# Kernel tuning notes

Measured on AMD Instinct MI355X. Metric: run time of the kernel, lower is better.

## Reference

```python
import jax, jax.numpy as jnp
import numpy as np

B, T = 32, 64
C, H, W = 1, 32, 32
A, E, D, S, HID = 2, 64, 128, 32, 128
K, STRIDE, PAD = 4, 2, 1
FEAT = 64 * 4 * 4  # conv stack output: 64 channels at 4x4


def _lin(x, w, b):
    return x @ w.T + b


def _conv(x, w, b):
    y = jax.lax.conv_general_dilated(x, w, (STRIDE, STRIDE), [(PAD, PAD)] * 2,
                                     dimension_numbers=('NCHW', 'OIHW', 'NCHW'))
    return y + b[None, :, None, None]


def _deconv(x, w, b):
    # torch ConvTranspose2d(w: (in_c,out_c,k,k), stride=2, pad=1) as dilated conv
    w_ = jnp.flip(w, (2, 3)).transpose(1, 0, 2, 3)
    p = K - 1 - PAD
    y = jax.lax.conv_general_dilated(x, w_, (1, 1), [(p, p)] * 2,
                                     lhs_dilation=(STRIDE, STRIDE),
                                     dimension_numbers=('NCHW', 'OIHW', 'NCHW'))
    return y + b[None, :, None, None]


def _mlp(x, w1, b1, w2, b2, w3, b3):
    h = jax.nn.elu(_lin(x, w1, b1))
    h = jax.nn.elu(_lin(h, w2, b2))
    out = _lin(h, w3, b3)
    return out[..., :S], jnp.clip(out[..., S:], -5.0, 2.0)


def _gru(x, h, wih, whh, bih, bhh):
    # torch nn.GRUCell semantics
    gi = x @ wih.T + bih
    gh = h @ whh.T + bhh
    ir, iz, inn = jnp.split(gi, 3, -1)
    hr, hz, hn = jnp.split(gh, 3, -1)
    r = jax.nn.sigmoid(ir + hr)
    u = jax.nn.sigmoid(iz + hz)
    n = jnp.tanh(inn + r * hn)
    return (1.0 - u) * n + u * h


def setup_inputs():
    keys = iter(jax.random.split(jax.random.key(0), 64))

    def p(shape, fan):
        return jax.random.normal(next(keys), shape, jnp.float32) / np.sqrt(fan)

    return dict(
        obs=jax.random.normal(next(keys), (B, T, C, H, W), jnp.float32),
        actions=jax.random.normal(next(keys), (B, T, A), jnp.float32),
        noise=jax.random.normal(next(keys), (T, B, S), jnp.float32),
        enc_w1=p((32, C, K, K), C * K * K), enc_b1=jnp.zeros(32),
        enc_w2=p((64, 32, K, K), 32 * K * K), enc_b2=jnp.zeros(64),
        enc_w3=p((64, 64, K, K), 64 * K * K), enc_b3=jnp.zeros(64),
        enc_pw=p((E, FEAT), FEAT), enc_pb=jnp.zeros(E),
        dec_pw=p((FEAT, D + S), D + S), dec_pb=jnp.zeros(FEAT),
        dec_w1=p((64, 64, K, K), 64 * K * K), dec_b1=jnp.zeros(64),
        dec_w2=p((64, 32, K, K), 64 * K * K), dec_b2=jnp.zeros(32),
        dec_w3=p((32, C, K, K), 32 * K * K), dec_b3=jnp.zeros(C),
        gru_wih=p((3 * D, S + A), D), gru_whh=p((3 * D, D), D),
        gru_bih=jnp.zeros(3 * D), gru_bhh=jnp.zeros(3 * D),
        pri_w1=p((HID, D + A), D + A), pri_b1=jnp.zeros(HID),
        pri_w2=p((HID, HID), HID), pri_b2=jnp.zeros(HID),
        pri_w3=p((2 * S, HID), HID), pri_b3=jnp.zeros(2 * S),
        pos_w1=p((HID, D + E), D + E), pos_b1=jnp.zeros(HID),
        pos_w2=p((HID, HID), HID), pos_b2=jnp.zeros(HID),
        pos_w3=p((2 * S, HID), HID), pos_b3=jnp.zeros(2 * S),
    )


def reference(obs, actions, noise, enc_w1, enc_b1, enc_w2, enc_b2, enc_w3, enc_b3,
              enc_pw, enc_pb, dec_pw, dec_pb, dec_w1, dec_b1, dec_w2, dec_b2,
              dec_w3, dec_b3, gru_wih, gru_whh, gru_bih, gru_bhh,
              pri_w1, pri_b1, pri_w2, pri_b2, pri_w3, pri_b3,
              pos_w1, pos_b1, pos_w2, pos_b2, pos_w3, pos_b3):
    Bq, Tq = obs.shape[:2]
    # --- CNN encoder over all frames at once ---
    x = obs.reshape(Bq * Tq, C, H, W)
    x = jax.nn.relu(_conv(x, enc_w1, enc_b1))
    x = jax.nn.relu(_conv(x, enc_w2, enc_b2))
    x = jax.nn.relu(_conv(x, enc_w3, enc_b3))
    embed = _lin(x.reshape(Bq * Tq, -1), enc_pw, enc_pb).reshape(Bq, Tq, E)

    # --- sequential RSSM core (use_posterior=True path) ---
    def step(h, inp):
        a, e_t, eps = inp
        pm, pls = _mlp(jnp.concatenate([h, e_t], -1),
                       pos_w1, pos_b1, pos_w2, pos_b2, pos_w3, pos_b3)
        z = pm + jnp.exp(pls) * eps
        prm, prls = _mlp(jnp.concatenate([h, a], -1),
                         pri_w1, pri_b1, pri_w2, pri_b2, pri_w3, pri_b3)
        h_new = _gru(jnp.concatenate([z, a], -1), h, gru_wih, gru_whh, gru_bih, gru_bhh)
        return h_new, (z, prm, prls, pm, pls, h)  # h = pre-update (used for decode)

    h0 = jnp.zeros((Bq, D), obs.dtype)
    h_final, (zs, prm, prls, pm, pls, hs) = jax.lax.scan(
        step, h0, (actions.swapaxes(0, 1), embed.swapaxes(0, 1), noise))

    # --- batched decode of all (h_t, z_t); same math as per-step decode ---
    hz = jnp.concatenate([hs, zs], -1).reshape(Tq * Bq, D + S)
    y = _lin(hz, dec_pw, dec_pb).reshape(Tq * Bq, 64, 4, 4)
    y = jax.nn.relu(_deconv(y, dec_w1, dec_b1))
    y = jax.nn.relu(_deconv(y, dec_w2, dec_b2))
    y = jax.nn.sigmoid(_deconv(y, dec_w3, dec_b3))
    recons = y.reshape(Tq, Bq, C, H, W).swapaxes(0, 1)

    tb = lambda t: t.swapaxes(0, 1)  # (T,B,.) -> (B,T,.)
    return (recons, tb(zs), tb(prm), tb(prls), tb(pm), tb(pls), h_final)
```

## Files before the change

### kernel.cpp

```cpp
#include <hip/hip_runtime.h>
#include <math.h>

#define NB 32
#define NT 64
#define NF 2048

#define OUT_ZS    2097152
#define OUT_PRM   (OUT_ZS + 65536)
#define OUT_PRLS  (OUT_PRM + 65536)
#define OUT_PM    (OUT_PRLS + 65536)
#define OUT_PLS   (OUT_PM + 65536)
#define OUT_HF    (OUT_PLS + 65536)

#define WS_HS    27394048
#define WS_ENCT  27656192
#define WS_DECT  27721728
#define WS_WP1H  27885568
#define WS_WP2   27893760
#define WS_WP3   27901952
#define WS_WWHH  27906048
#define WS_WIHZ  27930624
#define WS_QW1T  27936768
#define WS_QW2T  27953408
#define WS_QW3T  27969792
#define WS_PW1T  27977984
#define WS_WIHT  28002560
#define WS_WC2   16777216
#define WS_WC3   (WS_WC2 + 16384)
#define WS_WD1   (WS_WC3 + 32768)
#define WS_WD2   (WS_WD1 + 32768)
#define WS_POSL1E 25165824
#define WS_GIA    (WS_POSL1E + 262144)

typedef __attribute__((ext_vector_type(8))) short short8;
typedef __attribute__((ext_vector_type(4))) float floatx4;
typedef _Float16 __attribute__((ext_vector_type(2))) half2v;
union U4S8 { uint4 u; short8 s; };
__device__ __forceinline__ short8 u2s(uint4 u) { U4S8 x; x.u = u; return x.s; }
__device__ __forceinline__ float eluf(float a) { return (a > 0.f) ? a : expm1f(a); }
__device__ __forceinline__ float sigm(float a) { return 1.f / (1.f + expf(-a)); }
__device__ __forceinline__ unsigned short f2bf(float f) {
  unsigned int u = __float_as_uint(f);
  u += 0x7fffu + ((u >> 16) & 1u);
  return (unsigned short)(u >> 16);
}
__device__ __forceinline__ unsigned short f2h(float f) {
  _Float16 h = (_Float16)f;
  return __builtin_bit_cast(unsigned short, h);
}
union UH2 { unsigned int u; half2v h; };
__device__ __forceinline__ half2v u2h(unsigned int u) { UH2 x; x.u = u; return x.h; }

__device__ __forceinline__ float fdot2w(half2v a, half2v b, float c) {
#if __has_builtin(__builtin_amdgcn_fdot2)
  return __builtin_amdgcn_fdot2(a, b, c, false);
#else
  return fmaf((float)a[0], (float)b[0], fmaf((float)a[1], (float)b[1], c));
#endif
}

union U4H2 { uint4 u; half2v h[4]; };
__device__ __forceinline__ void dot8h(uint4 w, uint4 x,
                                      float& a0, float& a1, float& a2, float& a3) {
  U4H2 W; W.u = w;
  U4H2 X; X.u = x;
  a0 = fdot2w(W.h[0], X.h[0], a0);
  a1 = fdot2w(W.h[1], X.h[1], a1);
  a2 = fdot2w(W.h[2], X.h[2], a2);
  a3 = fdot2w(W.h[3], X.h[3], a3);
}

struct PP { const float* src; void* dst; int n; int mode; int A; int B; };
struct PPAll { PP m[16]; };

__global__ __launch_bounds__(256) void k_prep(PPAll a) {
  PP p = a.m[blockIdx.y];
  for (int i = blockIdx.x * 256 + threadIdx.x; i < p.n; i += gridDim.x * 256) {
    if (p.mode == 10) {
      const int r = i / p.B, c = i - r * p.B;
      ((float*)p.dst)[c * p.A + r] = p.src[i];
    } else {
      float v;
      if (p.mode == 0) v = p.src[i];
      else if (p.mode == 1) v = p.src[(i >> 7) * 192 + (i & 127)];
      else if (p.mode == 2) v = p.src[(i >> 5) * 34 + (i & 31)];
      else if (p.mode == 5) {
        const int kq = i >> 12, o = (i >> 2) & 1023, kl = (i >> 1) & 1, h = i & 1;
        v = p.src[o * 160 + kq * 4 + kl * 2 + h];
      } else {
        const int ab = p.A * p.B;
        const int t = i / ab, rem = i - t * ab;
        const int oc = rem / p.B, ic = rem - oc * p.B;
        v = (p.mode == 3) ? p.src[(oc * p.B + ic) * 16 + t]
                          : p.src[(ic * p.A + oc) * 16 + t];
      }
      ((unsigned short*)p.dst)[i] = (p.mode <= 2 || p.mode == 5) ? f2h(v) : f2bf(v);
    }
  }
}

__global__ __launch_bounds__(256, 2) void k_enc(
    const float* __restrict__ obs, const float* __restrict__ act,
    const float* __restrict__ w1, const float* __restrict__ b1,
    const unsigned short* __restrict__ wc2, const float* __restrict__ b2,
    const unsigned short* __restrict__ wc3, const float* __restrict__ b3,
    const float* __restrict__ encT, const float* __restrict__ encb,
    const float* __restrict__ pw1T, const float* __restrict__ pb1,
    const float* __restrict__ wihT, const float* __restrict__ bih,
    float* __restrict__ posl1e, float* __restrict__ gia) {
  const int f = blockIdx.x, tid = threadIdx.x;
  const int w = tid >> 6, l = tid & 63, q = l >> 4, n = l & 15;
  __shared__ float sIn1[32 * 33];
  __shared__ float sW1[512];
  __shared__ float sB1[32];
  __shared__ __align__(16) unsigned short sIn2[18 * 18 * 40];
  __shared__ __align__(16) unsigned short sIn3[10 * 10 * 72];
  __shared__ __align__(16) float sXe[1024];
  __shared__ float sP[256];
  __shared__ float sE[64];
  __shared__ float sA2[2];

  {
    const float* in = obs + (size_t)f * 1024;
    for (int i = tid; i < 1024; i += 256) sIn1[(i >> 5) * 33 + (i & 31)] = in[i];
    for (int i = tid; i < 512; i += 256) sW1[i] = w1[i];
    if (tid < 32) sB1[tid] = b1[tid];
    if (tid < 2) sA2[tid] = act[(size_t)f * 2 + tid];
    unsigned int* z2 = (unsigned int*)sIn2;
    for (int i = tid; i < 18 * 18 * 40 / 2; i += 256) z2[i] = 0u;
    unsigned int* z3 = (unsigned int*)sIn3;
    for (int i = tid; i < 10 * 10 * 72 / 2; i += 256) z3[i] = 0u;
  }
  __syncthreads();
  for (int r = tid; r < 512; r += 256) {
    const int oc = r >> 4, oy = r & 15;
    float acc[16];
    const float bv = sB1[oc];
#pragma unroll
    for (int j = 0; j < 16; j++) acc[j] = bv;
#pragma unroll
    for (int ky = 0; ky < 4; ky++) {
      const int iy = 2 * oy + ky - 1;
      if (iy < 0 || iy >= 32) continue;
#pragma unroll
      for (int kx = 0; kx < 4; kx++) {
        const float wv = sW1[oc * 16 + ky * 4 + kx];
#pragma unroll
        for (int j = 0; j < 16; j++) {
          const int ix = 2 * j + kx - 1;
          if (ix >= 0 && ix < 32) acc[j] += wv * sIn1[iy * 33 + ix];
        }
      }
    }
#pragma unroll
    for (int j = 0; j < 16; j++)
      sIn2[((oy + 1) * 18 + (j + 1)) * 40 + oc] = f2bf(fmaxf(acc[j], 0.f));
  }
  __syncthreads();
  {
    int base[4];
#pragma unroll
    for (int nt = 0; nt < 4; nt++) {
      const int px = nt * 16 + n, oy = px >> 3, ox = px & 7;
      base[nt] = ((2 * oy + 1) * 18 + (2 * ox + 1)) * 40 + q * 8;
    }
    floatx4 acc[4];
#pragma unroll
    for (int nt = 0; nt < 4; nt++) acc[nt] = (floatx4){0.f, 0.f, 0.f, 0.f};
    uint4 af[16];
#pragma unroll
    for (int t = 0; t < 16; t++)
      af[t] = *reinterpret_cast<const uint4*>(wc2 + (size_t)(t * 64 + w * 16 + n) * 32 + q * 8);
#pragma unroll
    for (int t = 0; t < 16; t++) {
      const int toff = ((t / 4 - 1) * 18 + (t % 4 - 1)) * 40;
#pragma unroll
      for (int nt = 0; nt < 4; nt++) {
        uint4 bf = *reinterpret_cast<const uint4*>(&sIn2[base[nt] + toff]);
        acc[nt] = __builtin_amdgcn_mfma_f32_16x16x32_bf16(u2s(af[t]), u2s(bf), acc[nt], 0, 0, 0);
      }
    }
    float b4[4];
#pragma unroll
    for (int r = 0; r < 4; r++) b4[r] = b2[w * 16 + q * 4 + r];
    __syncthreads();
#pragma unroll
    for (int nt = 0; nt < 4; nt++) {
      const int px = nt * 16 + n, oy = px >> 3, ox = px & 7;
#pragma unroll
      for (int r = 0; r < 4; r++)
        sIn3[((oy + 1) * 10 + (ox + 1)) * 72 + (w * 16 + q * 4 + r)] =
            f2bf(fmaxf(acc[nt][r] + b4[r], 0.f));
    }
  }
  __syncthreads();
  {
    const int oy = n >> 2, ox = n & 3;
    const int ibase = ((2 * oy + 1) * 10 + (2 * ox + 1)) * 72 + q * 8;
    floatx4 acc = (floatx4){0.f, 0.f, 0.f, 0.f};
    for (int ks = 0; ks < 2; ks++) {
      uint4 af[16];
#pragma unroll
      for (int t = 0; t < 16; t++)
        af[t] = *reinterpret_cast<const uint4*>(
            wc3 + (size_t)(t * 64 + w * 16 + n) * 64 + ks * 32 + q * 8);
#pragma unroll
      for (int t = 0; t < 16; t++) {
        const int toff = ((t / 4 - 1) * 10 + (t % 4 - 1)) * 72 + ks * 32;
        uint4 bf = *reinterpret_cast<const uint4*>(&sIn3[ibase + toff]);
        acc = __builtin_amdgcn_mfma_f32_16x16x32_bf16(u2s(af[t]), u2s(bf), acc, 0, 0, 0);
      }
    }
#pragma unroll
    for (int r = 0; r < 4; r++) {
      const int ch = w * 16 + q * 4 + r;
      sXe[ch * 16 + n] = fmaxf(acc[r] + b3[ch], 0.f);
    }
  }
  __syncthreads();
  {
    const int o = tid & 63, s = tid >> 6;
    float acc = 0.f;
    const int k0 = s * 256;
    for (int k = k0; k < k0 + 256; k++) acc += encT[k * 64 + o] * sXe[k];
    sP[tid] = acc;
  }
  __syncthreads();
  if (tid < 64)
    sE[tid] = sP[tid] + sP[tid + 64] + sP[tid + 128] + sP[tid + 192] + encb[tid];
  __syncthreads();
  if (tid < 128) {
    float a = pb1[tid];
    for (int k = 0; k < 64; k++) a += pw1T[(128 + k) * 128 + tid] * sE[k];
    posl1e[(size_t)f * 128 + tid] = a;
  } else {
#pragma unroll
    for (int jj = 0; jj < 3; jj++) {
      const int j = (tid - 128) + jj * 128;
      gia[(size_t)f * 384 + j] =
          bih[j] + wihT[32 * 384 + j] * sA2[0] + wihT[33 * 384 + j] * sA2[1];
    }
  }
}

__global__ __launch_bounds__(512, 2) void k_rssm4(
    const float* __restrict__ posl1e, const float* __restrict__ gia,
    const float* __restrict__ noise,
    const unsigned short* __restrict__ wp1h, const unsigned short* __restrict__ wp2,
    const unsigned short* __restrict__ wp3, const unsigned short* __restrict__ wwhh,
    const unsigned short* __restrict__ wihz,
    const float* __restrict__ pb2, const float* __restrict__ pb3,
    const float* __restrict__ bhh,
    float* __restrict__ hs, float* __restrict__ out) {
  const int b = blockIdx.x, tid = threadIdx.x;
  __shared__ __align__(16) _Float16 sHh[128];
  __shared__ __align__(16) _Float16 sL1h[128];
  __shared__ __align__(16) _Float16 sL2h[128];
  __shared__ __align__(16) _Float16 sZh[32];
  __shared__ float sGh[384];
  __shared__ float sPM[64];

  uint4 wA[16];
  {
    const unsigned short* rowA =
        (tid < 128) ? (wp1h + tid * 128) : (wwhh + (size_t)(tid - 128) * 128);
#pragma unroll
    for (int i = 0; i < 16; i++) wA[i] = reinterpret_cast<const uint4*>(rowA)[i];
  }
  uint4 wB[4];
  {
    const unsigned short* rowB = wp2 + (tid >> 2) * 128 + (tid & 3) * 32;
#pragma unroll
    for (int i = 0; i < 4; i++) wB[i] = reinterpret_cast<const uint4*>(rowB)[i];
  }
  uint4 wC[2];
  {
    const unsigned short* rowC = wp3 + (tid >> 3) * 128 + (tid & 7) * 16;
#pragma unroll
    for (int i = 0; i < 2; i++) wC[i] = reinterpret_cast<const uint4*>(rowC)[i];
  }
  uint4 wD[3][4];
  if (tid < 128) {
#pragma unroll
    for (int j = 0; j < 3; j++) {
      const unsigned short* rowD = wihz + (size_t)(tid + 128 * j) * 32;
#pragma unroll
      for (int i = 0; i < 4; i++) wD[j][i] = reinterpret_cast<const uint4*>(rowD)[i];
    }
  }
  const float bhhR = (tid >= 128) ? bhh[tid - 128] : 0.f;
  const float pb2R = pb2[tid >> 2];
  const float pb3mR = (tid < 32) ? pb3[tid] : 0.f;
  const float pb3sR = (tid < 32) ? pb3[tid + 32] : 0.f;

  float h_reg = 0.f;
  float pl1R = 0.f, gaR0 = 0.f, gaR1 = 0.f, gaR2 = 0.f, epsR = 0.f;
  if (tid < 128) {
    pl1R = posl1e[(size_t)(b * 64) * 128 + tid];
    const size_t gb = (size_t)(b * 64) * 384 + tid;
    gaR0 = gia[gb];
    gaR1 = gia[gb + 128];
    gaR2 = gia[gb + 256];
    sHh[tid] = (_Float16)0.f;
    hs[(size_t)b * 128 + tid] = 0.f;
  }
  if (tid < 32) epsR = noise[(size_t)b * 32 + tid];
  __syncthreads();

  for (int t = 0; t < 64; ++t) {
    const int tn = (t < 63) ? t + 1 : 63;
    float pl1N = 0.f, gaN0 = 0.f, gaN1 = 0.f, gaN2 = 0.f, epsN = 0.f;
    if (tid < 128) {
      pl1N = posl1e[(size_t)(b * 64 + tn) * 128 + tid];
      const size_t gb = (size_t)(b * 64 + tn) * 384 + tid;
      gaN0 = gia[gb];
      gaN1 = gia[gb + 128];
      gaN2 = gia[gb + 256];
    }
    if (tid < 32) epsN = noise[(size_t)(tn * 32 + b) * 32 + tid];

    {
      float a0 = 0.f, a1 = 0.f, a2 = 0.f, a3 = 0.f;
      const uint4* xs = reinterpret_cast<const uint4*>(sHh);
#pragma unroll
      for (int g = 0; g < 16; g++) dot8h(wA[g], xs[g], a0, a1, a2, a3);
      const float a = (a0 + a1) + (a2 + a3);
      if (tid < 128) sL1h[tid] = (_Float16)eluf(a + pl1R);
      else sGh[tid - 128] = a + bhhR;
    }
    __syncthreads();
    {
      float a0 = 0.f, a1 = 0.f, a2 = 0.f, a3 = 0.f;
      const uint4* xs = reinterpret_cast<const uint4*>(sL1h) + (tid & 3) * 4;
#pragma unroll
      for (int i = 0; i < 4; i++) dot8h(wB[i], xs[i], a0, a1, a2, a3);
      float p = (a0 + a1) + (a2 + a3);
      p += __shfl_xor(p, 1);
      p += __shfl_xor(p, 2);
      if ((tid & 3) == 0) sL2h[tid >> 2] = (_Float16)eluf(p + pb2R);
    }
    __syncthreads();
    {
      float a0 = 0.f, a1 = 0.f, a2 = 0.f, a3 = 0.f;
      const uint4* xs = reinterpret_cast<const uint4*>(sL2h) + (tid & 7) * 2;
      dot8h(wC[0], xs[0], a0, a1, a2, a3);
      dot8h(wC[1], xs[1], a0, a1, a2, a3);
      float p = (a0 + a1) + (a2 + a3);
      p += __shfl_xor(p, 1);
      p += __shfl_xor(p, 2);
      p += __shfl_xor(p, 4);
      if ((tid & 7) == 0) sPM[tid >> 3] = p;
    }
    __syncthreads();
    if (tid < 32) {
      const float pm = sPM[tid] + pb3mR;
      float pls = sPM[32 + tid] + pb3sR;
      pls = fminf(fmaxf(pls, -5.f), 2.f);
      const float z = pm + expf(pls) * epsR;
      sZh[tid] = (_Float16)z;
      const int o = (b * 64 + t) * 32 + tid;
      out[OUT_ZS + o] = z;
      out[OUT_PM + o] = pm;
      out[OUT_PLS + o] = pls;
    }
    __syncthreads();
    if (tid < 128) {
      float r0 = 0.f, r1 = 0.f, r2 = 0.f, r3 = 0.f;
      float u0 = 0.f, u1 = 0.f, u2 = 0.f, u3 = 0.f;
      float m0 = 0.f, m1 = 0.f, m2 = 0.f, m3 = 0.f;
      const uint4* xs = reinterpret_cast<const uint4*>(sZh);
#pragma unroll
      for (int i = 0; i < 4; i++) {
        const uint4 xv = xs[i];
        dot8h(wD[0][i], xv, r0, r1, r2, r3);
        dot8h(wD[1][i], xv, u0, u1, u2, u3);
        dot8h(wD[2][i], xv, m0, m1, m2, m3);
      }
      const float gr = gaR0 + ((r0 + r1) + (r2 + r3));
      const float gu = gaR1 + ((u0 + u1) + (u2 + u3));
      const float gn = gaR2 + ((m0 + m1) + (m2 + m3));
      const float r = sigm(gr + sGh[tid]);
      const float u = sigm(gu + sGh[128 + tid]);
      const float n = tanhf(gn + r * sGh[256 + tid]);
      const float hn = (1.f - u) * n + u * h_reg;
      h_reg = hn;
      sHh[tid] = (_Float16)hn;
      if (t < 63) hs[(size_t)((t + 1) * 32 + b) * 128 + tid] = hn;
    }
    pl1R = pl1N;
    gaR0 = gaN0;
    gaR1 = gaN1;
    gaR2 = gaN2;
    epsR = epsN;
    __syncthreads();
  }
  if (tid < 128) out[OUT_HF + b * 128 + tid] = h_reg;
}

__global__ __launch_bounds__(128) void k_pri(const float* __restrict__ hs,
    const float* __restrict__ act,
    const float* __restrict__ qw1T, const float* __restrict__ qb1,
    const float* __restrict__ qw2T, const float* __restrict__ qb2,
    const float* __restrict__ qw3T, const float* __restrict__ qb3,
    float* __restrict__ out) {
  __shared__ float sV[128], sW[128];
  __shared__ float sA2[2];
  const int f = blockIdx.x, tid = threadIdx.x;
  const int t = f >> 5, b = f & 31;
  sV[tid] = hs[(size_t)f * 128 + tid];
  if (tid < 2) sA2[tid] = act[(size_t)(b * 64 + t) * 2 + tid];
  __syncthreads();
  {
    float a = qb1[tid];
    for (int k = 0; k < 128; k++) a += qw1T[k * 128 + tid] * sV[k];
    a += qw1T[128 * 128 + tid] * sA2[0] + qw1T[129 * 128 + tid] * sA2[1];
    sW[tid] = eluf(a);
  }
  __syncthreads();
  {
    float a = qb2[tid];
    for (int k = 0; k < 128; k++) a += qw2T[k * 128 + tid] * sW[k];
    sV[tid] = eluf(a);
  }
  __syncthreads();
  if (tid < 64) {
    float a = qb3[tid];
    for (int k = 0; k < 128; k++) a += qw3T[k * 64 + tid] * sV[k];
    const int o = (b * 64 + t) * 32;
    if (tid < 32) out[OUT_PRM + o + tid] = a;
    else out[OUT_PRLS + o + tid - 32] = fminf(fmaxf(a, -5.f), 2.f);
  }
}

__global__ __launch_bounds__(256, 4) void k_dec(
    const float* __restrict__ hs, const float* __restrict__ zs,
    const unsigned short* __restrict__ decTh, const float* __restrict__ decb,
    const unsigned short* __restrict__ wd1, const float* __restrict__ db1,
    const unsigned short* __restrict__ wd2, const float* __restrict__ db2,
    const float* __restrict__ w3, const float* __restrict__ b3,
    float* __restrict__ out) {
  const int f = blockIdx.x, tid = threadIdx.x;
  const int w = tid >> 6, l = tid & 63, q = l >> 4, n = l & 15;
  const int t = f >> 5, b = f & 31;
  __shared__ __align__(16) _Float16 sXh[160];
  __shared__ __align__(16) unsigned short sInD1[6 * 6 * 72];
  __shared__ __align__(16) unsigned short sInD2[10 * 10 * 72];
  __shared__ __align__(16) _Float16 sInD3h[16 * 16 * 32];
  __shared__ __align__(16) _Float16 sW3h[16 * 32];

  if (tid < 128) sXh[tid] = (_Float16)hs[(size_t)f * 128 + tid];
  else if (tid < 160) sXh[tid] = (_Float16)zs[(size_t)(b * 64 + t) * 32 + (tid - 128)];
  {
    unsigned int* z1 = (unsigned int*)sInD1;
    for (int i = tid; i < 6 * 6 * 72 / 2; i += 256) z1[i] = 0u;
    unsigned int* z2 = (unsigned int*)sInD2;
    for (int i = tid; i < 10 * 10 * 72 / 2; i += 256) z2[i] = 0u;
    for (int s = tid; s < 512; s += 256) {
      const int tap = s >> 5, icc = s & 31;
      sW3h[s] = (_Float16)w3[icc * 16 + tap];
    }
  }
  __syncthreads();
  {
    float acA[4] = {0.f, 0.f, 0.f, 0.f};
    float acB[4] = {0.f, 0.f, 0.f, 0.f};
    const uint2* dT = reinterpret_cast<const uint2*>(decTh);
    const unsigned int* xh = reinterpret_cast<const unsigned int*>(sXh);
#pragma unroll 2
    for (int kq = 0; kq < 40; kq++) {
      const half2v x0 = u2h(xh[2 * kq]);
      const half2v x1 = u2h(xh[2 * kq + 1]);
#pragma unroll
      for (int i = 0; i < 4; i++) {
        const uint2 wv = dT[kq * 1024 + i * 256 + tid];
        acA[i] = fdot2w(u2h(wv.x), x0, acA[i]);
        acB[i] = fdot2w(u2h(wv.y), x1, acB[i]);
      }
    }
#pragma unroll
    for (int i = 0; i < 4; i++) {
      const int o = i * 256 + tid, c = o >> 4, px = o & 15;
      const int Y = px >> 2, X = px & 3;
      sInD1[((Y + 1) * 6 + (X + 1)) * 72 + c] = f2bf(acA[i] + acB[i] + decb[o]);
    }
  }
  __syncthreads();
  {
    const int Y = n >> 2, X = n & 3;
    const int ibase = ((Y + 1) * 6 + (X + 1)) * 72 + q * 8;
    float b4[4];
#pragma unroll
    for (int r = 0; r < 4; r++) b4[r] = db1[w * 16 + q * 4 + r];
#pragma unroll
    for (int c = 0; c < 4; c++) {
      const int cy = c >> 1, cx = c & 1;
      floatx4 acc = (floatx4){0.f, 0.f, 0.f, 0.f};
      for (int ks = 0; ks < 2; ks++) {
        uint4 af[4];
#pragma unroll
        for (int tt = 0; tt < 4; tt++) {
          const int t2 = tt >> 1, t3 = tt & 1;
          const int ky = ((cy + 1) & 1) + 2 * t2, kx = ((cx + 1) & 1) + 2 * t3;
          af[tt] = *reinterpret_cast<const uint4*>(
              wd1 + (size_t)((ky * 4 + kx) * 64 + w * 16 + n) * 64 + ks * 32 + q * 8);
        }
#pragma unroll
        for (int tt = 0; tt < 4; tt++) {
          const int t2 = tt >> 1, t3 = tt & 1;
          const int toff = ((cy - t2) * 6 + (cx - t3)) * 72 + ks * 32;
          uint4 bf = *reinterpret_cast<const uint4*>(&sInD1[ibase + toff]);
          acc = __builtin_amdgcn_mfma_f32_16x16x32_bf16(u2s(af[tt]), u2s(bf), acc, 0, 0, 0);
        }
      }
      const int oy = 2 * Y + cy, ox = 2 * X + cx;
#pragma unroll
      for (int r = 0; r < 4; r++)
        sInD2[((oy + 1) * 10 + (ox + 1)) * 72 + (w * 16 + q * 4 + r)] =
            f2bf(fmaxf(acc[r] + b4[r], 0.f));
    }
  }
  __syncthreads();
  {
    const int px = w * 16 + n;
    const int Y = px >> 3, X = px & 7;
    const int ibase = ((Y + 1) * 10 + (X + 1)) * 72 + q * 8;
    float b4[2][4];
#pragma unroll
    for (int mi = 0; mi < 2; mi++)
#pragma unroll
      for (int r = 0; r < 4; r++) b4[mi][r] = db2[mi * 16 + q * 4 + r];
#pragma unroll
    for (int c = 0; c < 4; c++) {
      const int cy = c >> 1, cx = c & 1;
      floatx4 acc[2];
      acc[0] = (floatx4){0.f, 0.f, 0.f, 0.f};
      acc[1] = (floatx4){0.f, 0.f, 0.f, 0.f};
      for (int ks = 0; ks < 2; ks++) {
        uint4 af[2][4];
#pragma unroll
        for (int mi = 0; mi < 2; mi++)
#pragma unroll
          for (int tt = 0; tt < 4; tt++) {
            const int t2 = tt >> 1, t3 = tt & 1;
            const int ky = ((cy + 1) & 1) + 2 * t2, kx = ((cx + 1) & 1) + 2 * t3;
            af[mi][tt] = *reinterpret_cast<const uint4*>(
                wd2 + (size_t)((ky * 4 + kx) * 32 + mi * 16 + n) * 64 + ks * 32 + q * 8);
          }
#pragma unroll
        for (int tt = 0; tt < 4; tt++) {
          const int t2 = tt >> 1, t3 = tt & 1;
          const int toff = ((cy - t2) * 10 + (cx - t3)) * 72 + ks * 32;
          uint4 bf = *reinterpret_cast<const uint4*>(&sInD2[ibase + toff]);
#pragma unroll
          for (int mi = 0; mi < 2; mi++)
            acc[mi] = __builtin_amdgcn_mfma_f32_16x16x32_bf16(u2s(af[mi][tt]), u2s(bf),
                                                              acc[mi], 0, 0, 0);
        }
      }
      const int oy = 2 * Y + cy, ox = 2 * X + cx;
#pragma unroll
      for (int mi = 0; mi < 2; mi++) {
        const unsigned int lo =
            (unsigned int)f2h(fmaxf(acc[mi][0] + b4[mi][0], 0.f)) |
            ((unsigned int)f2h(fmaxf(acc[mi][1] + b4[mi][1], 0.f)) << 16);
        const unsigned int hi =
            (unsigned int)f2h(fmaxf(acc[mi][2] + b4[mi][2], 0.f)) |
            ((unsigned int)f2h(fmaxf(acc[mi][3] + b4[mi][3], 0.f)) << 16);
        *reinterpret_cast<uint2*>(&sInD3h[(oy * 16 + ox) * 32 + mi * 16 + q * 4]) =
            make_uint2(lo, hi);
      }
    }
  }
  __syncthreads();
  {
    const int oy = tid >> 3;
    const int rem2 = tid & 7;
    const int cpar = rem2 >> 2, qq = rem2 & 3;
    const int py = (oy + 1) & 1, pc = (cpar + 1) & 1;
    float acc[4] = {0.f, 0.f, 0.f, 0.f};
    const float bv = b3[0];
#pragma unroll
    for (int u2 = 0; u2 < 2; u2++) {
      const int ky = py + 2 * u2;
      const int iy = (oy + 1 - ky) >> 1;
      if (iy < 0 || iy >= 16) continue;
#pragma unroll
      for (int u3 = 0; u3 < 2; u3++) {
        const int kx = pc + 2 * u3;
        const int ixb = (cpar + 1 - kx) >> 1;
        const uint4* wv = reinterpret_cast<const uint4*>(&sW3h[(ky * 4 + kx) * 32]);
        const uint4 w0 = wv[0], w1 = wv[1], w2 = wv[2], w3v = wv[3];
#pragma unroll
        for (int j = 0; j < 4; j++) {
          const int ix = ixb + qq * 4 + j;
          if (ix < 0 || ix >= 16) continue;
          const uint4* xp = reinterpret_cast<const uint4*>(&sInD3h[(iy * 16 + ix) * 32]);
          float a0 = 0.f, a1 = 0.f, a2 = 0.f, a3 = 0.f;
          dot8h(w0, xp[0], a0, a1, a2, a3);
          dot8h(w1, xp[1], a0, a1, a2, a3);
          dot8h(w2, xp[2], a0, a1, a2, a3);
          dot8h(w3v, xp[3], a0, a1, a2, a3);
          acc[j] += (a0 + a1) + (a2 + a3);
        }
      }
    }
    const int fo = b * 64 + t;
    float* yf = out + (size_t)fo * 1024;
#pragma unroll
    for (int j = 0; j < 4; j++)
      yf[oy * 32 + (cpar + 2 * (qq * 4 + j))] = 1.f / (1.f + expf(-(acc[j] + bv)));
  }
}

extern "C" void kernel_launch(void* const* d_in, const int* in_sizes, int n_in,
                              void* d_out, int out_size, void* d_ws, size_t ws_size,
                              hipStream_t stream) {
  const float* obs = (const float*)d_in[0];
  const float* actions = (const float*)d_in[1];
  const float* noise = (const float*)d_in[2];
  const float* enc_w1 = (const float*)d_in[3];
  const float* enc_b1 = (const float*)d_in[4];
  const float* enc_w2 = (const float*)d_in[5];
  const float* enc_b2 = (const float*)d_in[6];
  const float* enc_w3 = (const float*)d_in[7];
  const float* enc_b3 = (const float*)d_in[8];
  const float* enc_pw = (const float*)d_in[9];
  const float* enc_pb = (const float*)d_in[10];
  const float* dec_pw = (const float*)d_in[11];
  const float* dec_pb = (const float*)d_in[12];
  const float* dec_w1 = (const float*)d_in[13];
  const float* dec_b1 = (const float*)d_in[14];
  const float* dec_w2 = (const float*)d_in[15];
  const float* dec_b2 = (const float*)d_in[16];
  const float* dec_w3 = (const float*)d_in[17];
  const float* dec_b3 = (const float*)d_in[18];
  const float* gru_wih = (const float*)d_in[19];
  const float* gru_whh = (const float*)d_in[20];
  const float* gru_bih = (const float*)d_in[21];
  const float* gru_bhh = (const float*)d_in[22];
  const float* pri_w1 = (const float*)d_in[23];
  const float* pri_b1 = (const float*)d_in[24];
  const float* pri_w2 = (const float*)d_in[25];
  const float* pri_b2 = (const float*)d_in[26];
  const float* pri_w3 = (const float*)d_in[27];
  const float* pri_b3 = (const float*)d_in[28];
  const float* pos_w1 = (const float*)d_in[29];
  const float* pos_b1 = (const float*)d_in[30];
  const float* pos_w2 = (const float*)d_in[31];
  const float* pos_b2 = (const float*)d_in[32];
  const float* pos_w3 = (const float*)d_in[33];
  const float* pos_b3 = (const float*)d_in[34];

  float* out = (float*)d_out;
  float* ws = (float*)d_ws;
  float* HS = ws + WS_HS;
  float* POSL1E = ws + WS_POSL1E;
  float* GIA = ws + WS_GIA;
  unsigned short* WP1H = (unsigned short*)(ws + WS_WP1H);
  unsigned short* WP2 = (unsigned short*)(ws + WS_WP2);
  unsigned short* WP3 = (unsigned short*)(ws + WS_WP3);
  unsigned short* WWHH = (unsigned short*)(ws + WS_WWHH);
  unsigned short* WIHZ = (unsigned short*)(ws + WS_WIHZ);
  unsigned short* WC2 = (unsigned short*)(ws + WS_WC2);
  unsigned short* WC3 = (unsigned short*)(ws + WS_WC3);
  unsigned short* WD1 = (unsigned short*)(ws + WS_WD1);
  unsigned short* WD2 = (unsigned short*)(ws + WS_WD2);
  unsigned short* DECTH = (unsigned short*)(ws + WS_DECT);

  PPAll pp;
  pp.m[0]  = {enc_pw, ws + WS_ENCT, 64 * 1024, 10, 64, 1024};
  pp.m[1]  = {dec_pw, DECTH, 160 * 1024, 5, 0, 0};
  pp.m[2]  = {pri_w1, ws + WS_QW1T, 128 * 130, 10, 128, 130};
  pp.m[3]  = {pri_w2, ws + WS_QW2T, 128 * 128, 10, 128, 128};
  pp.m[4]  = {pri_w3, ws + WS_QW3T, 64 * 128, 10, 64, 128};
  pp.m[5]  = {pos_w1, ws + WS_PW1T, 128 * 192, 10, 128, 192};
  pp.m[6]  = {gru_wih, ws + WS_WIHT, 384 * 34, 10, 384, 34};
  pp.m[7]  = {pos_w1, WP1H, 128 * 128, 1, 0, 0};
  pp.m[8]  = {pos_w2, WP2, 128 * 128, 0, 0, 0};
  pp.m[9]  = {pos_w3, WP3, 64 * 128, 0, 0, 0};
  pp.m[10] = {gru_whh, WWHH, 384 * 128, 0, 0, 0};
  pp.m[11] = {gru_wih, WIHZ, 384 * 32, 2, 0, 0};
  pp.m[12] = {enc_w2, WC2, 16 * 64 * 32, 3, 64, 32};
  pp.m[13] = {enc_w3, WC3, 16 * 64 * 64, 3, 64, 64};
  pp.m[14] = {dec_w1, WD1, 16 * 64 * 64, 4, 64, 64};
  pp.m[15] = {dec_w2, WD2, 16 * 32 * 64, 4, 32, 64};
  hipLaunchKernelGGL(k_prep, dim3(32, 16), dim3(256), 0, stream, pp);

  k_enc<<<NF, 256, 0, stream>>>(obs, actions, enc_w1, enc_b1, WC2, enc_b2,
                                WC3, enc_b3, ws + WS_ENCT, enc_pb,
                                ws + WS_PW1T, pos_b1, ws + WS_WIHT, gru_bih,
                                POSL1E, GIA);

  k_rssm4<<<NB, 512, 0, stream>>>(POSL1E, GIA, noise, WP1H, WP2, WP3, WWHH, WIHZ,
                                  pos_b2, pos_b3, gru_bhh, HS, out);
  k_pri<<<NF, 128, 0, stream>>>(HS, actions, ws + WS_QW1T, pri_b1,
                                ws + WS_QW2T, pri_b2, ws + WS_QW3T, pri_b3, out);

  k_dec<<<NF, 256, 0, stream>>>(HS, out + OUT_ZS, DECTH, dec_pb,
                                WD1, dec_b1, WD2, dec_b2, dec_w3, dec_b3, out);
}
```

Before: 481.0 us.

## Fuse latent sampling into layer-3 shuffle reduction and pad decoder deconv3 LDS layout

In the recurrent kernel, the wp3 rows are interleaved so that the mean and log-std outputs for the same latent land in neighbouring 8-lane groups. One extra xor-shuffle then pairs them, which removes the sPM shared buffer and one __syncthreads per timestep on the serial critical path. In the decoder, the last deconv's input tile is padded per pixel and per row to cut LDS bank conflicts. Its inner loop is restructured to reuse 5 loaded pixels across 4 outputs and both kx taps, using packed dot2 in chunks of 4 channels. Boundary handling now loads zeros instead of skipping, which adds a few redundant FMAs.

```diff
diff --git a/kernel.cpp b/kernel.cpp
--- a/kernel.cpp
+++ b/kernel.cpp
@@ -258,7 +258,6 @@
   __shared__ __align__(16) _Float16 sL2h[128];
   __shared__ __align__(16) _Float16 sZh[32];
   __shared__ float sGh[384];
-  __shared__ float sPM[64];
 
   uint4 wA[16];
   {
@@ -275,7 +274,9 @@
   }
   uint4 wC[2];
   {
-    const unsigned short* rowC = wp3 + (tid >> 3) * 128 + (tid & 7) * 16;
+    const int r = tid >> 3;
+    const int o = (r >> 1) + ((r & 1) << 5);
+    const unsigned short* rowC = wp3 + o * 128 + (tid & 7) * 16;
 #pragma unroll
     for (int i = 0; i < 2; i++) wC[i] = reinterpret_cast<const uint4*>(rowC)[i];
   }
@@ -288,10 +289,12 @@
       for (int i = 0; i < 4; i++) wD[j][i] = reinterpret_cast<const uint4*>(rowD)[i];
     }
   }
+  const bool zlane = (tid & 15) == 0;
+  const int jz = tid >> 4;
   const float bhhR = (tid >= 128) ? bhh[tid - 128] : 0.f;
   const float pb2R = pb2[tid >> 2];
-  const float pb3mR = (tid < 32) ? pb3[tid] : 0.f;
-  const float pb3sR = (tid < 32) ? pb3[tid + 32] : 0.f;
+  const float pb3mR = zlane ? pb3[jz] : 0.f;
+  const float pb3sR = zlane ? pb3[jz + 32] : 0.f;
 
   float h_reg = 0.f;
   float pl1R = 0.f, gaR0 = 0.f, gaR1 = 0.f, gaR2 = 0.f, epsR = 0.f;
@@ -304,7 +307,7 @@
     sHh[tid] = (_Float16)0.f;
     hs[(size_t)b * 128 + tid] = 0.f;
   }
-  if (tid < 32) epsR = noise[(size_t)b * 32 + tid];
+  if (zlane) epsR = noise[(size_t)b * 32 + jz];
   __syncthreads();
 
   for (int t = 0; t < 64; ++t) {
@@ -317,7 +320,7 @@
       gaN1 = gia[gb + 128];
       gaN2 = gia[gb + 256];
     }
-    if (tid < 32) epsN = noise[(size_t)(tn * 32 + b) * 32 + tid];
+    if (zlane) epsN = noise[(size_t)(tn * 32 + b) * 32 + jz];
 
     {
       float a0 = 0.f, a1 = 0.f, a2 = 0.f, a3 = 0.f;
@@ -349,19 +352,18 @@
       p += __shfl_xor(p, 1);
       p += __shfl_xor(p, 2);
       p += __shfl_xor(p, 4);
-      if ((tid & 7) == 0) sPM[tid >> 3] = p;
-    }
-    __syncthreads();
-    if (tid < 32) {
-      const float pm = sPM[tid] + pb3mR;
-      float pls = sPM[32 + tid] + pb3sR;
-      pls = fminf(fmaxf(pls, -5.f), 2.f);
-      const float z = pm + expf(pls) * epsR;
-      sZh[tid] = (_Float16)z;
-      const int o = (b * 64 + t) * 32 + tid;
-      out[OUT_ZS + o] = z;
-      out[OUT_PM + o] = pm;
-      out[OUT_PLS + o] = pls;
+      const float pq = __shfl_xor(p, 8);
+      if (zlane) {
+        const float pm = p + pb3mR;
+        float pls = pq + pb3sR;
+        pls = fminf(fmaxf(pls, -5.f), 2.f);
+        const float z = pm + expf(pls) * epsR;
+        sZh[jz] = (_Float16)z;
+        const int o = (b * 64 + t) * 32 + jz;
+        out[OUT_ZS + o] = z;
+        out[OUT_PM + o] = pm;
+        out[OUT_PLS + o] = pls;
+      }
     }
     __syncthreads();
     if (tid < 128) {
@@ -432,6 +434,8 @@
   }
 }
 
+#define D3_ROW 580
+#define D3_PX  36
 __global__ __launch_bounds__(256, 4) void k_dec(
     const float* __restrict__ hs, const float* __restrict__ zs,
     const unsigned short* __restrict__ decTh, const float* __restrict__ decb,
@@ -445,7 +449,7 @@
   __shared__ __align__(16) _Float16 sXh[160];
   __shared__ __align__(16) unsigned short sInD1[6 * 6 * 72];
   __shared__ __align__(16) unsigned short sInD2[10 * 10 * 72];
-  __shared__ __align__(16) _Float16 sInD3h[16 * 16 * 32];
+  __shared__ __align__(16) _Float16 sInD3h[16 * D3_ROW];
   __shared__ __align__(16) _Float16 sW3h[16 * 32];
 
   if (tid < 128) sXh[tid] = (_Float16)hs[(size_t)f * 128 + tid];
@@ -566,7 +570,7 @@
         const unsigned int hi =
             (unsigned int)f2h(fmaxf(acc[mi][2] + b4[mi][2], 0.f)) |
             ((unsigned int)f2h(fmaxf(acc[mi][3] + b4[mi][3], 0.f)) << 16);
-        *reinterpret_cast<uint2*>(&sInD3h[(oy * 16 + ox) * 32 + mi * 16 + q * 4]) =
+        *reinterpret_cast<uint2*>(&sInD3h[oy * D3_ROW + ox * D3_PX + mi * 16 + q * 4]) =
             make_uint2(lo, hi);
       }
     }
@@ -577,6 +581,8 @@
     const int rem2 = tid & 7;
     const int cpar = rem2 >> 2, qq = rem2 & 3;
     const int py = (oy + 1) & 1, pc = (cpar + 1) & 1;
+    const int ixb0 = (cpar + 1 - pc) >> 1;
+    const int xlo = ixb0 - 1 + qq * 4;
     float acc[4] = {0.f, 0.f, 0.f, 0.f};
     const float bv = b3[0];
 #pragma unroll
@@ -584,23 +590,26 @@
       const int ky = py + 2 * u2;
       const int iy = (oy + 1 - ky) >> 1;
       if (iy < 0 || iy >= 16) continue;
-#pragma unroll
-      for (int u3 = 0; u3 < 2; u3++) {
-        const int kx = pc + 2 * u3;
-        const int ixb = (cpar + 1 - kx) >> 1;
-        const uint4* wv = reinterpret_cast<const uint4*>(&sW3h[(ky * 4 + kx) * 32]);
-        const uint4 w0 = wv[0], w1 = wv[1], w2 = wv[2], w3v = wv[3];
+      const _Float16* rowp = &sInD3h[iy * D3_ROW];
+      const uint2* wAp = reinterpret_cast<const uint2*>(&sW3h[(ky * 4 + pc) * 32]);
+      const uint2* wBp = reinterpret_cast<const uint2*>(&sW3h[(ky * 4 + pc + 2) * 32]);
+#pragma unroll
+      for (int kb = 0; kb < 8; kb++) {
+        uint2 xv[5];
+#pragma unroll
+        for (int x = 0; x < 5; x++) {
+          const int ix = xlo + x;
+          xv[x] = (ix >= 0 && ix < 16)
+              ? *reinterpret_cast<const uint2*>(&rowp[ix * D3_PX + kb * 4])
+              : make_uint2(0u, 0u);
+        }
+        const uint2 wa = wAp[kb], wb = wBp[kb];
 #pragma unroll
         for (int j = 0; j < 4; j++) {
-          const int ix = ixb + qq * 4 + j;
-          if (ix < 0 || ix >= 16) continue;
-          const uint4* xp = reinterpret_cast<const uint4*>(&sInD3h[(iy * 16 + ix) * 32]);
-          float a0 = 0.f, a1 = 0.f, a2 = 0.f, a3 = 0.f;
-          dot8h(w0, xp[0], a0, a1, a2, a3);
-          dot8h(w1, xp[1], a0, a1, a2, a3);
-          dot8h(w2, xp[2], a0, a1, a2, a3);
-          dot8h(w3v, xp[3], a0, a1, a2, a3);
-          acc[j] += (a0 + a1) + (a2 + a3);
+          acc[j] = fdot2w(u2h(wa.x), u2h(xv[j + 1].x), acc[j]);
+          acc[j] = fdot2w(u2h(wa.y), u2h(xv[j + 1].y), acc[j]);
+          acc[j] = fdot2w(u2h(wb.x), u2h(xv[j].x), acc[j]);
+          acc[j] = fdot2w(u2h(wb.y), u2h(xv[j].y), acc[j]);
         }
       }
     }
```

Result: no change. 474.5 us (-1.4%).
